# Performance work log

Hardware: AMD Instinct MI355X
Metric: run time of the kernel (lower is better)

The kernel has to match this reference:

```python
import jax, jax.numpy as jnp
import numpy as np

EPS = 1e-6
NEG = -100000.0


def _ln(x):
    # LayerNorm, elementwise_affine=False, eps=1e-6
    mu = jnp.mean(x, axis=-1, keepdims=True)
    var = jnp.mean((x - mu) ** 2, axis=-1, keepdims=True)
    return (x - mu) * jax.lax.rsqrt(var + EPS)


def _split_heads(x, h):
    b, s, d = x.shape
    return x.reshape(b, s, h, d // h).transpose(0, 2, 1, 3)  # [B,H,S,Dh]


def _merge_heads(x):
    b, h, s, dh = x.shape
    return x.transpose(0, 2, 1, 3).reshape(b, s, h * dh)


def _conv_pool(x, w):
    # grouped Conv2d(num_heads -> num_heads, kernel=(4,1), stride=(4,1), groups=num_heads, bias=False)
    # x: [B,H,S,Dh] as NCHW, w: [H,1,4,1] as OIHW
    return jax.lax.conv_general_dilated(
        x, w, window_strides=(4, 1), padding='VALID',
        dimension_numbers=('NCHW', 'OIHW', 'NCHW'),
        feature_group_count=x.shape[1])


def setup_inputs() -> dict:
    key = jax.random.key(0)
    ks = jax.random.split(key, 14)
    B, S, M, D, QKV, MLP, H = 4, 4096, 256, 768, 768, 3072, 12
    std = 0.02
    f = lambda k, shp: jax.random.normal(k, shp, jnp.float32) * std
    return {
        'x': jax.random.normal(ks[0], (B, S, D), jnp.float32),
        'memory': jax.random.normal(ks[1], (B, M, D), jnp.float32),
        'mask': jax.random.randint(ks[2], (B, S), 0, 2).astype(jnp.int32),
        'Wq': f(ks[3], (QKV, D)), 'Wk': f(ks[4], (QKV, D)),
        'Wv': f(ks[5], (QKV, D)), 'Wo': f(ks[6], (D, QKV)),
        'conv_w': f(ks[7], (H, 1, 4, 1)),
        'Uq': f(ks[8], (QKV, D)), 'Uk': f(ks[9], (QKV, D)),
        'Uv': f(ks[10], (QKV, D)), 'Uo': f(ks[11], (D, QKV)),
        'W1': f(ks[12], (MLP, D)), 'W2': f(ks[13], (D, MLP)),
    }


def reference(x, memory, mask, Wq, Wk, Wv, Wo, conv_w, Uq, Uk, Uv, Uo, W1, W2):
    H = conv_w.shape[0]
    maskf = mask.astype(x.dtype)                       # [B,S]

    # ---- pack: ConvAttention(memory as q, x as k/v); conv downsamples k/v ->
    #      shape_change=True so the k_mask is skipped (as in the torch code).
    q = _split_heads(memory @ Wq.T, H)                 # [B,H,M,Dh], unit temperature (log_temp=0)
    k = _split_heads(x @ Wk.T, H)                      # [B,H,S,Dh]
    v = _split_heads(x @ Wv.T, H)
    k = _conv_pool(k, conv_w)                          # [B,H,S//4,Dh]
    v = _conv_pool(v, conv_w)
    logits = jnp.einsum('bhqd,bhkd->bhqk', q, k)
    att = jax.nn.softmax(logits, axis=-1)
    packed = _merge_heads(att @ v) @ Wo.T              # [B,M,D]

    # ---- unpack: TAttention(x as q, packed as k/v) with q_mask injection
    head_dim = Uq.shape[0] // H
    uq = _split_heads(x @ Uq.T, H) * (1.0 / jnp.sqrt(jnp.asarray(head_dim, x.dtype)))
    uk = _split_heads(packed @ Uk.T, H)                # [B,H,M,Dh]
    uv = _split_heads(packed @ Uv.T, H)
    ulogits = jnp.einsum('bhqd,bhkd->bhqk', uq, uk)    # [B,H,S,M]
    ulogits = ulogits + NEG * (1.0 - maskf[:, None, :, None])
    uatt = jax.nn.softmax(ulogits, axis=-1)
    unpacked = _merge_heads(uatt @ uv) @ Uo.T          # [B,S,D]

    unpacked = unpacked * maskf[..., None]
    q_out = _ln(x + unpacked)
    m_out = _ln(memory + packed)

    # FFN: Linear -> GELU(exact) -> Linear (dropout=0)
    h = jax.nn.gelu(jnp.einsum('bsd,md->bsm', q_out, W1), approximate=False)
    y = jnp.einsum('bsm,dm->bsd', h, W2)
    y = y * maskf[..., None]
    q_out = _ln(q_out + y)
    return (q_out, m_out)
```

## Files before the change

kernel.cpp:

```cpp
#include <hip/hip_runtime.h>
#include <hip/hip_bf16.h>
#include <math.h>


typedef unsigned short u16;
typedef __attribute__((ext_vector_type(8))) short bf8v;
typedef __attribute__((ext_vector_type(4))) float f4v;
typedef __attribute__((ext_vector_type(4))) unsigned short us4v;

#define AS1 __attribute__((address_space(1)))
#define AS3 __attribute__((address_space(3)))

__device__ __forceinline__ void gld_lds16(const void* g, void* l) {
  __builtin_amdgcn_global_load_lds((const AS1 unsigned int*)g,
                                   (AS3 unsigned int*)l, 16, 0, 0);
}

__device__ __forceinline__ u16 bf16_rne(float x) {
  unsigned u = __float_as_uint(x);
  return (u16)((u + 0x7fffu + ((u >> 16) & 1u)) >> 16);
}
__device__ __forceinline__ float bf16_to_f(u16 h) {
  return __uint_as_float(((unsigned)h) << 16);
}

struct Cvt8 {
  const float* src[8];
  u16* dst[8];
  int n4[8];
  float sc[8];
  int cum[9];
  int ns;
};
__global__ __launch_bounds__(256) void tobf16_multi_kernel(Cvt8 c) {
  int b = blockIdx.x;
  int seg = 0;
  while (seg + 1 < c.ns && b >= c.cum[seg + 1]) ++seg;
  int i = (b - c.cum[seg]) * 256 + threadIdx.x;
  if (i >= c.n4[seg]) return;
  const float sc = c.sc[seg];
  float4 v = ((const float4*)c.src[seg])[i];
  us4v h;
  h[0] = bf16_rne(v.x * sc); h[1] = bf16_rne(v.y * sc);
  h[2] = bf16_rne(v.z * sc); h[3] = bf16_rne(v.w * sc);
  ((us4v*)c.dst[seg])[i] = h;
}

template <int BN, int GELU, int OMODE>
__global__ __launch_bounds__(256) void bgemm_kernel(
    const u16* __restrict__ A, const u16* __restrict__ B,
    float* __restrict__ Cf, u16* __restrict__ Cb, int M, int N, int K,
    int lda, int ldb, int ldc, long long aSB, long long aSH, long long bSB,
    long long bSH, long long cSB, long long cSH, int HB, float scale) {
  constexpr int NJ = BN / 32;
  constexpr int LPB = BN / 64;
  __shared__ u16 smA[3][4096];
  __shared__ u16 smB[3][BN * 32];
  const int t = threadIdx.x;
  const int w = t >> 6, lane = t & 63;
  const int z = blockIdx.z;
  const int bb = z / HB, hh = z % HB;
  const u16* Ab = A + bb * aSB + hh * aSH;
  const u16* Bb = B + bb * bSB + hh * bSH;
  float* Cfb = (OMODE != 1) ? (Cf + bb * cSB + hh * cSH) : nullptr;
  u16* Cbb = (OMODE >= 1) ? (Cb + bb * cSB + hh * cSH) : nullptr;

  const int gx = gridDim.x;
  const int nwg = gx * gridDim.y;
  int f = blockIdx.x + gx * blockIdx.y;
  if ((nwg & 7) == 0) {
    const int cpx = nwg >> 3;
    f = (f & 7) * cpx + (f >> 3);
  }
  const int row0 = (f / gx) * 128, col0 = (f % gx) * BN;

  const int brow_l = lane >> 2;
  const int bchunk = ((lane & 3) ^ ((lane >> 3) & 3)) * 8;
  const int fr = lane & 15;
  const int fq = lane >> 4;
  const int fco = (fq ^ ((lane >> 1) & 3)) * 8;
  const int wr = (w >> 1) * 64, wc = (w & 1) * (BN / 2);

  f4v acc[4][NJ];
#pragma unroll
  for (int i = 0; i < 4; ++i)
#pragma unroll
    for (int j = 0; j < NJ; ++j) acc[i][j] = {0.f, 0.f, 0.f, 0.f};

  const int NT = K >> 5;

  auto stage = [&](int tile, int buf) {
    const int k0 = tile << 5;
#pragma unroll
    for (int i = 0; i < 2; ++i) {
      const int g = w * 2 + i;
      const int r = g * 16 + brow_l;
      gld_lds16(Ab + (long long)(row0 + r) * lda + k0 + bchunk,
                &smA[buf][g * 512 + lane * 8]);
    }
#pragma unroll
    for (int i = 0; i < LPB; ++i) {
      const int g = w * LPB + i;
      const int r = g * 16 + brow_l;
      gld_lds16(Bb + (long long)(col0 + r) * ldb + k0 + bchunk,
                &smB[buf][g * 512 + lane * 8]);
    }
  };
#define WAIT_L()                                            \
  do {                                                      \
    if constexpr (BN == 128)                                \
      asm volatile("s_waitcnt vmcnt(4)" ::: "memory");      \
    else                                                    \
      asm volatile("s_waitcnt vmcnt(3)" ::: "memory");      \
  } while (0)

  stage(0, 0);
  if (NT > 1) {
    stage(1, 1);
    WAIT_L();
  } else {
    asm volatile("s_waitcnt vmcnt(0)" ::: "memory");
  }
  __builtin_amdgcn_sched_barrier(0);
  __builtin_amdgcn_s_barrier();

  int cur = 0;
  for (int tt = 0; tt < NT; ++tt) {
    const int nn2 = (cur + 2 >= 3) ? cur - 1 : cur + 2;
    if (tt + 2 < NT) stage(tt + 2, nn2);
    {
      bf8v af[4], bfr[NJ];
#pragma unroll
      for (int mi = 0; mi < 4; ++mi)
        af[mi] = *(const bf8v*)&smA[cur][(wr + mi * 16 + fr) * 32 + fco];
#pragma unroll
      for (int nj = 0; nj < NJ; ++nj)
        bfr[nj] = *(const bf8v*)&smB[cur][(wc + nj * 16 + fr) * 32 + fco];
      __builtin_amdgcn_s_setprio(1);
#pragma unroll
      for (int mi = 0; mi < 4; ++mi)
#pragma unroll
        for (int nj = 0; nj < NJ; ++nj)
          acc[mi][nj] = __builtin_amdgcn_mfma_f32_16x16x32_bf16(
              af[mi], bfr[nj], acc[mi][nj], 0, 0, 0);
      __builtin_amdgcn_s_setprio(0);
    }
    if (tt + 2 < NT) {
      WAIT_L();
    } else if (tt + 1 < NT) {
      asm volatile("s_waitcnt vmcnt(0)" ::: "memory");
    }
    __builtin_amdgcn_sched_barrier(0);
    __builtin_amdgcn_s_barrier();
    cur = (cur + 1 >= 3) ? 0 : cur + 1;
  }
#undef WAIT_L

#pragma unroll
  for (int mi = 0; mi < 4; ++mi)
#pragma unroll
    for (int nj = 0; nj < NJ; ++nj) {
      const int col = col0 + wc + nj * 16 + fr;
      const long long base =
          (long long)(row0 + wr + mi * 16 + fq * 4) * ldc + col;
#pragma unroll
      for (int j = 0; j < 4; ++j) {
        float v = acc[mi][nj][j] * scale;
        if (GELU) v = 0.5f * v * (1.f + erff(v * 0.70710678118654752f));
        const long long idx = base + (long long)j * ldc;
        if (OMODE != 1) Cfb[idx] = v;
        if (OMODE >= 1) Cbb[idx] = bf16_rne(v);
      }
    }
}

__global__ __launch_bounds__(512) void fused_pack_attn(
    const u16* __restrict__ q, const u16* __restrict__ k,
    const u16* __restrict__ vt, u16* __restrict__ o) {
  __shared__ char pool[110080];
  u16* smQ = (u16*)pool;
  u16* smK = (u16*)(pool + 16384);
  u16* Pbuf = (u16*)(pool + 32768);
  u16* smV = (u16*)(pool + 98304);
  float* partial = (float*)(pool + 106496);
  float* mold = (float*)(pool + 108544);
  float* fbuf = (float*)(pool + 109056);
  float* srow = (float*)(pool + 109568);

  const int t = threadIdx.x;
  const int w = t >> 6, lane = t & 63;
  const int z = blockIdx.z;
  const int b = z / 12, h = z % 12;
  const int qrow0 = b * 256 + blockIdx.x * 128;
  const long long kvbase = ((long long)(b * 12 + h)) * 65536;

  const int fr = lane & 15, fq = lane >> 4;
  const int fco = (fq ^ ((lane >> 1) & 3)) * 8;
  const int brow_l = lane >> 2;
  const int bchunk = ((lane & 3) ^ ((lane >> 3) & 3)) * 8;
  const int wr = (w >> 2) * 64, wc = (w & 3) * 64;
  const int wrp = (w >> 1) * 32, wcp = (w & 1) * 32;

#pragma unroll
  for (int i = 0; i < 2; ++i) {
    const int g = w * 2 + i;
    const int plane = g >> 3, grp = g & 7;
    gld_lds16(q + (long long)(qrow0 + grp * 16 + brow_l) * 768 + h * 64 +
                  plane * 32 + bchunk,
              smQ + plane * 4096 + grp * 512 + lane * 8);
  }
  if (t < 128) {
    mold[t] = -3.0e38f;
    srow[t] = 0.f;
  }

  f4v acc2[2][2];
#pragma unroll
  for (int i = 0; i < 2; ++i)
#pragma unroll
    for (int j = 0; j < 2; ++j) acc2[i][j] = {0.f, 0.f, 0.f, 0.f};

  for (int kc = 0; kc < 4; ++kc) {
    f4v acc[4][4];
#pragma unroll
    for (int i = 0; i < 4; ++i)
#pragma unroll
      for (int j = 0; j < 4; ++j) acc[i][j] = {0.f, 0.f, 0.f, 0.f};

#pragma unroll
    for (int khalf = 0; khalf < 2; ++khalf) {
      __syncthreads();
#pragma unroll
      for (int i = 0; i < 2; ++i) {
        const int g = w * 2 + i;
        gld_lds16(k + kvbase +
                      (long long)(kc * 256 + g * 16 + brow_l) * 64 +
                      khalf * 32 + bchunk,
                  smK + g * 512 + lane * 8);
      }
      __syncthreads();
#pragma unroll
      for (int mi = 0; mi < 4; ++mi) {
        const bf8v a0 =
            *(const bf8v*)&smQ[khalf * 4096 + (wr + mi * 16 + fr) * 32 + fco];
#pragma unroll
        for (int nj = 0; nj < 4; ++nj) {
          const bf8v b0 = *(const bf8v*)&smK[(wc + nj * 16 + fr) * 32 + fco];
          acc[mi][nj] =
              __builtin_amdgcn_mfma_f32_16x16x32_bf16(a0, b0, acc[mi][nj], 0, 0, 0);
        }
      }
    }
    __syncthreads();

#pragma unroll
    for (int mi = 0; mi < 4; ++mi)
#pragma unroll
      for (int j = 0; j < 4; ++j) {
        float m = fmaxf(fmaxf(acc[mi][0][j], acc[mi][1][j]),
                        fmaxf(acc[mi][2][j], acc[mi][3][j]));
#pragma unroll
        for (int o2 = 1; o2 < 16; o2 <<= 1) m = fmaxf(m, __shfl_xor(m, o2));
        if (fr == 0) partial[(w & 3) * 128 + wr + mi * 16 + fq * 4 + j] = m;
      }
    __syncthreads();
    if (t < 128) {
      const float cm = fmaxf(fmaxf(partial[t], partial[128 + t]),
                             fmaxf(partial[256 + t], partial[384 + t]));
      const float mnew = fmaxf(mold[t], cm);
      fbuf[t] = exp2f(mold[t] - mnew);
      mold[t] = mnew;
    }
    __syncthreads();

#pragma unroll
    for (int mi = 0; mi < 4; ++mi)
#pragma unroll
      for (int j = 0; j < 4; ++j) {
        const int row = wr + mi * 16 + fq * 4 + j;
        const float rm = mold[row];
        float s = 0.f;
#pragma unroll
        for (int nj = 0; nj < 4; ++nj) {
          const float e = exp2f(acc[mi][nj][j] - rm);
          s += e;
          const int col = wc + nj * 16 + fr;
          const int kc2 = col >> 5, kloc = col & 31;
          Pbuf[kc2 * 4096 + row * 32 + (((kloc >> 3) ^ ((row >> 1) & 3)) * 8) +
               (kloc & 7)] = bf16_rne(e);
        }
#pragma unroll
        for (int o2 = 1; o2 < 16; o2 <<= 1) s += __shfl_xor(s, o2);
        if (fr == 0) partial[(w & 3) * 128 + row] = s;
      }
    if (w < 4) {
      gld_lds16(vt + kvbase + (long long)(w * 16 + brow_l) * 1024 + kc * 256 +
                    bchunk,
                smV + w * 512 + lane * 8);
    }
    __syncthreads();
    if (t < 128)
      srow[t] = srow[t] * fbuf[t] +
                ((partial[t] + partial[128 + t]) +
                 (partial[256 + t] + partial[384 + t]));
    __syncthreads();

#pragma unroll
    for (int mi = 0; mi < 2; ++mi)
#pragma unroll
      for (int j = 0; j < 4; ++j) {
        const float fr_ = fbuf[wrp + mi * 16 + fq * 4 + j];
        acc2[mi][0][j] *= fr_;
        acc2[mi][1][j] *= fr_;
      }

    for (int sk = 0; sk < 8; ++sk) {
      const int cur = (sk & 1) * 2048;
      if (sk < 7 && w < 4) {
        gld_lds16(vt + kvbase + (long long)(w * 16 + brow_l) * 1024 +
                      kc * 256 + (sk + 1) * 32 + bchunk,
                  smV + (2048 - cur) + w * 512 + lane * 8);
      }
#pragma unroll
      for (int mi = 0; mi < 2; ++mi) {
        const bf8v pa =
            *(const bf8v*)&Pbuf[sk * 4096 + (wrp + mi * 16 + fr) * 32 + fco];
#pragma unroll
        for (int nj = 0; nj < 2; ++nj) {
          const bf8v v0 =
              *(const bf8v*)&smV[cur + (wcp + nj * 16 + fr) * 32 + fco];
          acc2[mi][nj] =
              __builtin_amdgcn_mfma_f32_16x16x32_bf16(pa, v0, acc2[mi][nj], 0, 0, 0);
        }
      }
      __syncthreads();
    }
  }

  if (t < 128) fbuf[t] = 1.f / srow[t];
  __syncthreads();
  const long long ooff = (long long)qrow0 * 768 + h * 64;
#pragma unroll
  for (int mi = 0; mi < 2; ++mi)
#pragma unroll
    for (int nj = 0; nj < 2; ++nj)
#pragma unroll
      for (int j = 0; j < 4; ++j) {
        const int row = wrp + mi * 16 + fq * 4 + j;
        const int col = wcp + nj * 16 + fr;
        o[ooff + (long long)row * 768 + col] =
            bf16_rne(acc2[mi][nj][j] * fbuf[row]);
      }
}

__global__ __launch_bounds__(512) void fused_unpack_attn(
    const u16* __restrict__ q, int ldq, const u16* __restrict__ k, int ldk,
    const u16* __restrict__ vt, u16* __restrict__ o) {
  __shared__ char pool[76800];
  u16* smA = (u16*)pool;
  u16* smB = (u16*)(pool + 8192);
  u16* Pbuf = (u16*)pool;
  u16* smV = (u16*)(pool + 65536);
  float* partial = (float*)(pool + 73728);
  float* rowmax = (float*)(pool + 75776);
  float* rowsum = (float*)(pool + 76288);

  const int t = threadIdx.x;
  const int w = t >> 6, lane = t & 63;
  const int z = blockIdx.z;
  const int b = z / 12, h = z % 12;
  const int q0 = blockIdx.x * 128;

  const long long qoff = (long long)(b * 4096 + q0) * ldq + h * 64;
  const long long koff = (long long)(b * 256) * ldk + h * 64;
  const long long vbase = ((long long)(b * 12 + h)) * 16384;
  const long long ooff = (long long)(b * 4096 + q0) * 768 + h * 64;

  const int fr = lane & 15, fq = lane >> 4;
  const int fco = (fq ^ ((lane >> 1) & 3)) * 8;
  const int brow_l = lane >> 2;
  const int bchunk = ((lane & 3) ^ ((lane >> 3) & 3)) * 8;

  const int wr = (w >> 2) * 64, wc = (w & 3) * 64;
  f4v acc[4][4];
#pragma unroll
  for (int i = 0; i < 4; ++i)
#pragma unroll
    for (int j = 0; j < 4; ++j) acc[i][j] = {0.f, 0.f, 0.f, 0.f};

  for (int k0 = 0; k0 < 64; k0 += 32) {
    __syncthreads();
#pragma unroll
    for (int i = 0; i < 2; ++i) {
      const int g = w * 2 + i;
      const int r = g * 16 + brow_l;
      gld_lds16(k + koff + (long long)r * ldk + k0 + bchunk,
                smB + g * 512 + lane * 8);
    }
    {
      const int r = w * 16 + brow_l;
      gld_lds16(q + qoff + (long long)r * ldq + k0 + bchunk,
                smA + w * 512 + lane * 8);
    }
    __syncthreads();
#pragma unroll
    for (int mi = 0; mi < 4; ++mi) {
      const bf8v a0 = *(const bf8v*)&smA[(wr + mi * 16 + fr) * 32 + fco];
#pragma unroll
      for (int nj = 0; nj < 4; ++nj) {
        const bf8v b0 = *(const bf8v*)&smB[(wc + nj * 16 + fr) * 32 + fco];
        acc[mi][nj] = __builtin_amdgcn_mfma_f32_16x16x32_bf16(a0, b0, acc[mi][nj], 0, 0, 0);
      }
    }
  }
  __syncthreads();

  if (w < 4) {
    const int r = w * 16 + brow_l;
    gld_lds16(vt + vbase + (long long)r * 256 + bchunk,
              smV + w * 512 + lane * 8);
  }

#pragma unroll
  for (int mi = 0; mi < 4; ++mi)
#pragma unroll
    for (int j = 0; j < 4; ++j) {
      float m = fmaxf(fmaxf(acc[mi][0][j], acc[mi][1][j]),
                      fmaxf(acc[mi][2][j], acc[mi][3][j]));
#pragma unroll
      for (int o2 = 1; o2 < 16; o2 <<= 1) m = fmaxf(m, __shfl_xor(m, o2));
      if (fr == 0) partial[(w & 3) * 128 + wr + mi * 16 + fq * 4 + j] = m;
    }
  __syncthreads();
  if (t < 128)
    rowmax[t] = fmaxf(fmaxf(partial[t], partial[128 + t]),
                      fmaxf(partial[256 + t], partial[384 + t]));
  __syncthreads();
#pragma unroll
  for (int mi = 0; mi < 4; ++mi)
#pragma unroll
    for (int j = 0; j < 4; ++j) {
      const int row = wr + mi * 16 + fq * 4 + j;
      const float rm = rowmax[row];
      float s = 0.f;
#pragma unroll
      for (int nj = 0; nj < 4; ++nj) {
        const float e = exp2f(acc[mi][nj][j] - rm);
        s += e;
        const int col = wc + nj * 16 + fr;
        const int kc = col >> 5, kloc = col & 31;
        Pbuf[kc * 4096 + row * 32 + (((kloc >> 3) ^ ((row >> 1) & 3)) * 8) +
             (kloc & 7)] = bf16_rne(e);
      }
#pragma unroll
      for (int o2 = 1; o2 < 16; o2 <<= 1) s += __shfl_xor(s, o2);
      if (fr == 0) partial[(w & 3) * 128 + row] = s;
    }
  __syncthreads();
  if (t < 128)
    rowsum[t] = 1.f / ((partial[t] + partial[128 + t]) +
                       (partial[256 + t] + partial[384 + t]));
  __syncthreads();

  const int wrp = (w >> 1) * 32, wcp = (w & 1) * 32;
  f4v acc2[2][2];
#pragma unroll
  for (int i = 0; i < 2; ++i)
#pragma unroll
    for (int j = 0; j < 2; ++j) acc2[i][j] = {0.f, 0.f, 0.f, 0.f};

  for (int kc = 0; kc < 8; ++kc) {
    const int cur = (kc & 1) * 2048;
    if (kc < 7 && w < 4) {
      const int r = w * 16 + brow_l;
      gld_lds16(vt + vbase + (long long)r * 256 + (kc + 1) * 32 + bchunk,
                smV + (2048 - cur) + w * 512 + lane * 8);
    }
#pragma unroll
    for (int mi = 0; mi < 2; ++mi) {
      const bf8v pa =
          *(const bf8v*)&Pbuf[kc * 4096 + (wrp + mi * 16 + fr) * 32 + fco];
#pragma unroll
      for (int nj = 0; nj < 2; ++nj) {
        const bf8v v0 =
            *(const bf8v*)&smV[cur + (wcp + nj * 16 + fr) * 32 + fco];
        acc2[mi][nj] = __builtin_amdgcn_mfma_f32_16x16x32_bf16(pa, v0, acc2[mi][nj], 0, 0, 0);
      }
    }
    __syncthreads();
  }
#pragma unroll
  for (int mi = 0; mi < 2; ++mi)
#pragma unroll
    for (int nj = 0; nj < 2; ++nj)
#pragma unroll
      for (int j = 0; j < 4; ++j) {
        const int row = wrp + mi * 16 + fq * 4 + j;
        const int col = wcp + nj * 16 + fr;
        o[ooff + (long long)row * 768 + col] =
            bf16_rne(acc2[mi][nj][j] * rowsum[row]);
      }
}

__global__ __launch_bounds__(256) void conv_bf16_kernel(
    const u16* __restrict__ in, const float* __restrict__ w,
    u16* __restrict__ o, int total, int ld) {
  int idx = blockIdx.x * 256 + threadIdx.x;
  if (idx >= total) return;
  const int dh = idx & 63;
  int r = idx >> 6;
  const int tt = r & 1023; r >>= 10;
  const int h = r % 12;
  const int b = r / 12;
  const long long s = ((long long)(b * 4096 + 4 * tt)) * ld + h * 64 + dh;
  const float* wh = w + h * 4;
  float v = 0.f;
#pragma unroll
  for (int j = 0; j < 4; ++j) v = fmaf(wh[j], bf16_to_f(in[s + j * ld]), v);
  o[idx] = bf16_rne(v);
}

__global__ __launch_bounds__(256) void convT_bf16_kernel(
    const u16* __restrict__ in, const float* __restrict__ w,
    u16* __restrict__ o, int total, int ld) {
  int idx = blockIdx.x * 256 + threadIdx.x;
  if (idx >= total) return;
  const int tt = idx & 1023;
  int r = idx >> 10;
  const int dh = r & 63; r >>= 6;
  const int h = r % 12;
  const int b = r / 12;
  const long long s = ((long long)(b * 4096 + 4 * tt)) * ld + h * 64 + dh;
  const float* wh = w + h * 4;
  float v = 0.f;
#pragma unroll
  for (int j = 0; j < 4; ++j) v = fmaf(wh[j], bf16_to_f(in[s + j * ld]), v);
  o[idx] = bf16_rne(v);
}

__global__ __launch_bounds__(256) void transT_b2b_kernel(
    const u16* __restrict__ in, u16* __restrict__ o, int total, int ld) {
  int idx = blockIdx.x * 256 + threadIdx.x;
  if (idx >= total) return;
  const int key = idx & 255;
  int r = idx >> 8;
  const int dh = r & 63; r >>= 6;
  const int h = r % 12;
  const int b = r / 12;
  o[idx] = in[((long long)(b * 256 + key)) * ld + h * 64 + dh];
}

template <int BBF16>
__global__ __launch_bounds__(256) void ln_kernel(
    const float* __restrict__ a, const float* __restrict__ bf,
    const u16* __restrict__ bb, const int* __restrict__ mask,
    float* __restrict__ out, u16* __restrict__ outb) {
  const long long row = blockIdx.x;
  const float* pa = a + row * 768;
  const float ms = mask ? (float)mask[row] : 1.f;
  __shared__ float buf[768];
  __shared__ float red[4];
  const int t = threadIdx.x;
  float lsum = 0.f;
#pragma unroll
  for (int i = t; i < 768; i += 256) {
    const float bvv = BBF16 ? bf16_to_f(bb[row * 768 + i]) : bf[row * 768 + i];
    const float v = fmaf(bvv, ms, pa[i]);
    buf[i] = v;
    lsum += v;
  }
  for (int o = 32; o; o >>= 1) lsum += __shfl_xor(lsum, o);
  if ((t & 63) == 0) red[t >> 6] = lsum;
  __syncthreads();
  const float mu = (red[0] + red[1] + red[2] + red[3]) * (1.f / 768.f);
  float lvar = 0.f;
#pragma unroll
  for (int i = t; i < 768; i += 256) {
    const float d = buf[i] - mu;
    lvar = fmaf(d, d, lvar);
  }
  __syncthreads();
  for (int o = 32; o; o >>= 1) lvar += __shfl_xor(lvar, o);
  if ((t & 63) == 0) red[t >> 6] = lvar;
  __syncthreads();
  const float var = (red[0] + red[1] + red[2] + red[3]) * (1.f / 768.f);
  const float rstd = rsqrtf(var + 1e-6f);
  float* po = out + row * 768;
  u16* pob = outb ? outb + row * 768 : nullptr;
#pragma unroll
  for (int i = t; i < 768; i += 256) {
    const float v = (buf[i] - mu) * rstd;
    po[i] = v;
    if (outb) pob[i] = bf16_rne(v);
  }
}

extern "C" void kernel_launch(void* const* d_in, const int* in_sizes, int n_in,
                              void* d_out, int out_size, void* d_ws,
                              size_t ws_size, hipStream_t stream) {
  const float* x = (const float*)d_in[0];
  const float* memory = (const float*)d_in[1];
  const int* mask = (const int*)d_in[2];
  const float* Wq = (const float*)d_in[3];
  const float* Wk = (const float*)d_in[4];
  const float* Wv = (const float*)d_in[5];
  const float* Wo = (const float*)d_in[6];
  const float* conv_w = (const float*)d_in[7];
  const float* Uq = (const float*)d_in[8];
  const float* Uk = (const float*)d_in[9];
  const float* Uv = (const float*)d_in[10];
  const float* Uo = (const float*)d_in[11];
  const float* W1 = (const float*)d_in[12];
  const float* W2 = (const float*)d_in[13];
  float* out = (float*)d_out;
  float* ws = (float*)d_ws;

  const int XR = 16384, MR = 1024, D = 768, MLP = 3072;
  const long long CB = 3145728;
  const int WD = 589824;
  const int WM = 2359296;

  float* A0 = ws + 0;
  float* A1 = ws + 18874368;
  float* A2 = ws + 31457280;

  u16* xb    = (u16*)(A0 + 12582912);
  u16* kvqb  = (u16*)A0;
  u16* uattvb = (u16*)A1;
  u16* unpb  = (u16*)A0;
  float* qout1 = A0 + 6291456;
  u16* qout1b = (u16*)(out + 6291456);
  u16* hb    = (u16*)A1;
  float* ybuf = A2;

  u16* kpb  = (u16*)A2;
  u16* vpTb = kpb + 3145728;
  u16* qpb  = (u16*)(A2 + 3145728);
  u16* memb = qpb + 786432;
  u16* avmb = (u16*)(A2 + 3932160);
  u16* pkb  = avmb + 786432;
  float* packed = A2 + 4718592;
  u16* ukvb = (u16*)(A2 + 5505024);
  u16* uvTb = (u16*)(A2 + 6291456);
  u16* wp16 = (u16*)(A2 + 7077888);

  u16* Wkvqb = wp16;
  u16* Wqb = wp16 + 2304 * 768;
  u16* Wob = Wqb + WD;
  u16* Ukvb2 = wp16;
  u16* Uob = wp16 + 1536 * 768;
  u16* W1b = wp16;
  u16* W2b = wp16 + WM;

  const float UQS = 0.18033688011112042592f;
  const float L2E = 1.4426950408889634074f;

  {
    Cvt8 c{};
    const float* ss[7] = {x, memory, Wk, Wv, Uq, Wq, Wo};
    u16* dd[7] = {xb, memb, Wkvqb, Wkvqb + WD, Wkvqb + 2 * WD, Wqb, Wob};
    int nn[7] = {3145728, 196608, WD / 4, WD / 4, WD / 4, WD / 4, WD / 4};
    float sc[7] = {1.f, 1.f, 1.f, 1.f, UQS, 1.f, 1.f};
    int cum = 0;
    for (int i = 0; i < 7; ++i) {
      c.src[i] = ss[i]; c.dst[i] = dd[i]; c.n4[i] = nn[i]; c.sc[i] = sc[i];
      c.cum[i] = cum; cum += (nn[i] + 255) / 256;
    }
    c.cum[7] = cum; c.ns = 7;
    tobf16_multi_kernel<<<cum, 256, 0, stream>>>(c);
  }
  bgemm_kernel<128, 0, 1><<<dim3(18, 128, 1), 256, 0, stream>>>(
      xb, Wkvqb, nullptr, kvqb, XR, 2304, D, D, D, 2304,
      0, 0, 0, 0, 0, 0, 1, 1.f);
  bgemm_kernel<128, 0, 1><<<dim3(6, 8, 1), 256, 0, stream>>>(
      memb, Wqb, nullptr, qpb, MR, D, D, D, D, D, 0, 0, 0, 0, 0, 0, 1, L2E);
  conv_bf16_kernel<<<12288, 256, 0, stream>>>(kvqb, conv_w, kpb, 3145728, 2304);
  convT_bf16_kernel<<<12288, 256, 0, stream>>>(kvqb + 768, conv_w, vpTb, 3145728, 2304);
  {
    dim3 g(2, 1, 48);
    fused_pack_attn<<<g, 512, 0, stream>>>(qpb, kpb, vpTb, avmb);
  }
  bgemm_kernel<128, 0, 2><<<dim3(6, 8, 1), 256, 0, stream>>>(
      avmb, Wob, packed, pkb, MR, D, D, D, D, D, 0, 0, 0, 0, 0, 0, 1, 1.f);
  ln_kernel<0><<<MR, 256, 0, stream>>>(memory, packed, nullptr, nullptr,
                                       out + 12582912, nullptr);

  {
    Cvt8 c{};
    const float* ss[3] = {Uk, Uv, Uo};
    u16* dd[3] = {Ukvb2, Ukvb2 + WD, Uob};
    int cum = 0;
    for (int i = 0; i < 3; ++i) {
      c.src[i] = ss[i]; c.dst[i] = dd[i]; c.n4[i] = WD / 4; c.sc[i] = 1.f;
      c.cum[i] = cum; cum += (WD / 4 + 255) / 256;
    }
    c.cum[3] = cum; c.ns = 3;
    tobf16_multi_kernel<<<cum, 256, 0, stream>>>(c);
  }
  bgemm_kernel<128, 0, 1><<<dim3(12, 8, 1), 256, 0, stream>>>(
      pkb, Ukvb2, nullptr, ukvb, MR, 1536, D, D, D, 1536,
      0, 0, 0, 0, 0, 0, 1, 1.f);
  transT_b2b_kernel<<<3072, 256, 0, stream>>>(ukvb + 768, uvTb, 786432, 1536);
  {
    dim3 g(32, 1, 48);
    fused_unpack_attn<<<g, 512, 0, stream>>>(kvqb + 1536, 2304, ukvb, 1536,
                                             uvTb, uattvb);
  }
  bgemm_kernel<128, 0, 1><<<dim3(6, 32, 4), 256, 0, stream>>>(
      uattvb, Uob, nullptr, unpb, 4096, D, D, D, D, D,
      CB, 0, 0, 0, CB, 0, 1, 1.f);
  ln_kernel<1><<<XR, 256, 0, stream>>>(x, nullptr, unpb, mask, qout1, qout1b);

  {
    Cvt8 c{};
    const float* ss[2] = {W1, W2};
    u16* dd[2] = {W1b, W2b};
    int cum = 0;
    for (int i = 0; i < 2; ++i) {
      c.src[i] = ss[i]; c.dst[i] = dd[i]; c.n4[i] = WM / 4; c.sc[i] = 1.f;
      c.cum[i] = cum; cum += (WM / 4 + 255) / 256;
    }
    c.cum[2] = cum; c.ns = 2;
    tobf16_multi_kernel<<<cum, 256, 0, stream>>>(c);
  }
  for (int c = 0; c < 2; ++c) {
    bgemm_kernel<128, 1, 1><<<dim3(24, 32, 2), 256, 0, stream>>>(
        qout1b + (long long)c * 2 * CB, W1b, nullptr, hb, 4096, MLP, D,
        D, D, MLP, CB, 0, 0, 0, 12582912, 0, 1, 1.f);
    bgemm_kernel<128, 0, 0><<<dim3(6, 32, 2), 256, 0, stream>>>(
        hb, W2b, ybuf, nullptr, 4096, D, MLP, MLP, MLP, D,
        12582912, 0, 0, 0, CB, 0, 1, 1.f);
    ln_kernel<0><<<8192, 256, 0, stream>>>(qout1 + (long long)c * 2 * CB, ybuf,
                                           nullptr, mask + c * 8192,
                                           out + (long long)c * 2 * CB, nullptr);
  }
}
```

Baseline: 687.2 us.

## Add 256-row GEMM tiles for large GEMMs and fuse K/V conv pooling

Adds a BM template parameter to the bf16 GEMM so the large projections (KVQ, Uo, W1) can run with 256x128 tiles and 512-thread blocks, raising operand reuse per block and halving the grid. It also merges the two conv-pooling kernels into one that reads the K and V slices together and writes K normally and V transposed. The larger tiles use more LDS and registers per block, which can lower occupancy. The transposed V store in the fused conv is uncoalesced.

After: 638.9 us, median of 2. 7.0% less time.

```diff
diff --git a/kernel.cpp b/kernel.cpp
--- a/kernel.cpp
+++ b/kernel.cpp
@@ -46,15 +46,17 @@
   ((us4v*)c.dst[seg])[i] = h;
 }
 
-template <int BN, int GELU, int OMODE>
-__global__ __launch_bounds__(256) void bgemm_kernel(
+template <int BM, int BN, int GELU, int OMODE>
+__global__ __launch_bounds__(BM * 2) void bgemm_kernel(
     const u16* __restrict__ A, const u16* __restrict__ B,
     float* __restrict__ Cf, u16* __restrict__ Cb, int M, int N, int K,
     int lda, int ldb, int ldc, long long aSB, long long aSH, long long bSB,
     long long bSH, long long cSB, long long cSH, int HB, float scale) {
   constexpr int NJ = BN / 32;
-  constexpr int LPB = BN / 64;
-  __shared__ u16 smA[3][4096];
+  constexpr int NW = BM / 32;
+  constexpr int LPB = (BN / 16) / NW;
+  constexpr int VW = 2 + LPB;
+  __shared__ u16 smA[3][BM * 32];
   __shared__ u16 smB[3][BN * 32];
   const int t = threadIdx.x;
   const int w = t >> 6, lane = t & 63;
@@ -72,7 +74,7 @@
     const int cpx = nwg >> 3;
     f = (f & 7) * cpx + (f >> 3);
   }
-  const int row0 = (f / gx) * 128, col0 = (f % gx) * BN;
+  const int row0 = (f / gx) * BM, col0 = (f % gx) * BN;
 
   const int brow_l = lane >> 2;
   const int bchunk = ((lane & 3) ^ ((lane >> 3) & 3)) * 8;
@@ -108,7 +110,7 @@
   };
 #define WAIT_L()                                            \
   do {                                                      \
-    if constexpr (BN == 128)                                \
+    if constexpr (VW == 4)                                  \
       asm volatile("s_waitcnt vmcnt(4)" ::: "memory");      \
     else                                                    \
       asm volatile("s_waitcnt vmcnt(3)" ::: "memory");      \
@@ -502,9 +504,9 @@
       }
 }
 
-__global__ __launch_bounds__(256) void conv_bf16_kernel(
+__global__ __launch_bounds__(256) void conv_dual_kernel(
     const u16* __restrict__ in, const float* __restrict__ w,
-    u16* __restrict__ o, int total, int ld) {
+    u16* __restrict__ ok, u16* __restrict__ ovT, int total, int ld) {
   int idx = blockIdx.x * 256 + threadIdx.x;
   if (idx >= total) return;
   const int dh = idx & 63;
@@ -514,28 +516,14 @@
   const int b = r / 12;
   const long long s = ((long long)(b * 4096 + 4 * tt)) * ld + h * 64 + dh;
   const float* wh = w + h * 4;
-  float v = 0.f;
-#pragma unroll
-  for (int j = 0; j < 4; ++j) v = fmaf(wh[j], bf16_to_f(in[s + j * ld]), v);
-  o[idx] = bf16_rne(v);
-}
-
-__global__ __launch_bounds__(256) void convT_bf16_kernel(
-    const u16* __restrict__ in, const float* __restrict__ w,
-    u16* __restrict__ o, int total, int ld) {
-  int idx = blockIdx.x * 256 + threadIdx.x;
-  if (idx >= total) return;
-  const int tt = idx & 1023;
-  int r = idx >> 10;
-  const int dh = r & 63; r >>= 6;
-  const int h = r % 12;
-  const int b = r / 12;
-  const long long s = ((long long)(b * 4096 + 4 * tt)) * ld + h * 64 + dh;
-  const float* wh = w + h * 4;
-  float v = 0.f;
-#pragma unroll
-  for (int j = 0; j < 4; ++j) v = fmaf(wh[j], bf16_to_f(in[s + j * ld]), v);
-  o[idx] = bf16_rne(v);
+  float vk = 0.f, vv = 0.f;
+#pragma unroll
+  for (int j = 0; j < 4; ++j) {
+    vk = fmaf(wh[j], bf16_to_f(in[s + j * ld]), vk);
+    vv = fmaf(wh[j], bf16_to_f(in[s + 768 + j * ld]), vv);
+  }
+  ok[idx] = bf16_rne(vk);
+  ovT[(((long long)(b * 12 + h)) * 64 + dh) * 1024 + tt] = bf16_rne(vv);
 }
 
 __global__ __launch_bounds__(256) void transT_b2b_kernel(
@@ -669,18 +657,18 @@
     c.cum[7] = cum; c.ns = 7;
     tobf16_multi_kernel<<<cum, 256, 0, stream>>>(c);
   }
-  bgemm_kernel<128, 0, 1><<<dim3(18, 128, 1), 256, 0, stream>>>(
+  bgemm_kernel<256, 128, 0, 1><<<dim3(18, 64, 1), 512, 0, stream>>>(
       xb, Wkvqb, nullptr, kvqb, XR, 2304, D, D, D, 2304,
       0, 0, 0, 0, 0, 0, 1, 1.f);
-  bgemm_kernel<128, 0, 1><<<dim3(6, 8, 1), 256, 0, stream>>>(
+  bgemm_kernel<128, 128, 0, 1><<<dim3(6, 8, 1), 256, 0, stream>>>(
       memb, Wqb, nullptr, qpb, MR, D, D, D, D, D, 0, 0, 0, 0, 0, 0, 1, L2E);
-  conv_bf16_kernel<<<12288, 256, 0, stream>>>(kvqb, conv_w, kpb, 3145728, 2304);
-  convT_bf16_kernel<<<12288, 256, 0, stream>>>(kvqb + 768, conv_w, vpTb, 3145728, 2304);
+  conv_dual_kernel<<<12288, 256, 0, stream>>>(kvqb, conv_w, kpb, vpTb,
+                                              3145728, 2304);
   {
     dim3 g(2, 1, 48);
     fused_pack_attn<<<g, 512, 0, stream>>>(qpb, kpb, vpTb, avmb);
   }
-  bgemm_kernel<128, 0, 2><<<dim3(6, 8, 1), 256, 0, stream>>>(
+  bgemm_kernel<128, 128, 0, 2><<<dim3(6, 8, 1), 256, 0, stream>>>(
       avmb, Wob, packed, pkb, MR, D, D, D, D, D, 0, 0, 0, 0, 0, 0, 1, 1.f);
   ln_kernel<0><<<MR, 256, 0, stream>>>(memory, packed, nullptr, nullptr,
                                        out + 12582912, nullptr);
@@ -697,7 +685,7 @@
     c.cum[3] = cum; c.ns = 3;
     tobf16_multi_kernel<<<cum, 256, 0, stream>>>(c);
   }
-  bgemm_kernel<128, 0, 1><<<dim3(12, 8, 1), 256, 0, stream>>>(
+  bgemm_kernel<128, 128, 0, 1><<<dim3(12, 8, 1), 256, 0, stream>>>(
       pkb, Ukvb2, nullptr, ukvb, MR, 1536, D, D, D, 1536,
       0, 0, 0, 0, 0, 0, 1, 1.f);
   transT_b2b_kernel<<<3072, 256, 0, stream>>>(ukvb + 768, uvTb, 786432, 1536);
@@ -706,7 +694,7 @@
     fused_unpack_attn<<<g, 512, 0, stream>>>(kvqb + 1536, 2304, ukvb, 1536,
                                              uvTb, uattvb);
   }
-  bgemm_kernel<128, 0, 1><<<dim3(6, 32, 4), 256, 0, stream>>>(
+  bgemm_kernel<256, 128, 0, 1><<<dim3(6, 16, 4), 512, 0, stream>>>(
       uattvb, Uob, nullptr, unpb, 4096, D, D, D, D, D,
       CB, 0, 0, 0, CB, 0, 1, 1.f);
   ln_kernel<1><<<XR, 256, 0, stream>>>(x, nullptr, unpb, mask, qout1, qout1b);
@@ -724,10 +712,10 @@
     tobf16_multi_kernel<<<cum, 256, 0, stream>>>(c);
   }
   for (int c = 0; c < 2; ++c) {
-    bgemm_kernel<128, 1, 1><<<dim3(24, 32, 2), 256, 0, stream>>>(
+    bgemm_kernel<256, 128, 1, 1><<<dim3(24, 16, 2), 512, 0, stream>>>(
         qout1b + (long long)c * 2 * CB, W1b, nullptr, hb, 4096, MLP, D,
         D, D, MLP, CB, 0, 0, 0, 12582912, 0, 1, 1.f);
-    bgemm_kernel<128, 0, 0><<<dim3(6, 32, 2), 256, 0, stream>>>(
+    bgemm_kernel<128, 128, 0, 0><<<dim3(6, 32, 2), 256, 0, stream>>>(
         hb, W2b, ybuf, nullptr, 4096, D, MLP, MLP, MLP, D,
         12582912, 0, 0, 0, CB, 0, 1, 1.f);
     ln_kernel<0><<<8192, 256, 0, stream>>>(qout1 + (long long)c * 2 * CB, ybuf,
```
